# Kernel optimization log

Hardware: AMD Instinct MI355X
Metric: run time of the kernel (lower is better)

Reference implementation:

```python
import jax, jax.numpy as jnp
import numpy as np

D_MODEL = 128
NEG_INF = -1e30


def setup_inputs() -> dict:
    key = jax.random.key(0)
    k1, k2, k3, k4 = jax.random.split(key, 4)
    B, Lc, Lq, d = 32, 2048, 256, D_MODEL
    C = jax.random.normal(k1, (B, Lc, d), dtype=jnp.float32)
    Q = jax.random.normal(k2, (B, Lq, d), dtype=jnp.float32)
    # Linear(3d, 1): weight laid out for cat order (Q_, C_, C_*Q_)
    w = jax.random.normal(k3, (3 * d,), dtype=jnp.float32) / np.sqrt(3 * d)
    b = jax.random.normal(k4, (1,), dtype=jnp.float32) * 0.01
    c_mask = jnp.ones((B, Lc), dtype=jnp.int32)
    q_mask = jnp.ones((B, Lq), dtype=jnp.int32)
    return {"C": C, "Q": Q, "w": w, "b": b, "c_mask": c_mask, "q_mask": q_mask}


def reference(C, Q, w, b, c_mask, q_mask):
    d = C.shape[-1]
    # Algebraic decomposition of Linear([Q_, C_, C_*Q_]) -> scalar:
    # S[b,i,j] = Q[b,j]@w_q + C[b,i]@w_c + (C[b,i]*w_m)@Q[b,j] + bias
    w_q, w_c, w_m = w[:d], w[d:2 * d], w[2 * d:]
    S = (C @ w_c)[:, :, None] \
        + (Q @ w_q)[:, None, :] \
        + jnp.einsum('bid,bjd->bij', C * w_m, Q) \
        + b[0]                                        # (B, Lc, Lq)
    mask = (c_mask[:, :, None] * q_mask[:, None, :]).astype(S.dtype)
    S = S * mask + NEG_INF * (1.0 - mask)
    S1 = jax.nn.softmax(S, axis=1)  # softmax over context dim (as in source)
    S2 = jax.nn.softmax(S, axis=2)  # softmax over query dim
    C2Q = jnp.einsum('bij,bjd->bid', S1, Q)           # (B, Lc, d)
    # Q2C = S1 @ S2^T @ C, associated as S1 @ (S2^T @ C) to avoid (Lc,Lc)
    T = jnp.einsum('bkj,bkd->bjd', S2, C)             # (B, Lq, d)
    Q2C = jnp.einsum('bij,bjd->bid', S1, T)           # (B, Lc, d)
    out = jnp.concatenate([C, C2Q, C * C2Q, C * Q2C], axis=2)  # (B, Lc, 4d)
    # dropout omitted (deterministic reference / eval mode)
    return out
```

## Files before the change

kernel.cpp:

```cpp
#include <hip/hip_runtime.h>


#define BB   32
#define LC   2048
#define LQ   256
#define DM   128
#define NEG_INF_F (-1e30f)

using bf16x8  = __attribute__((ext_vector_type(8))) __bf16;
using f32x4   = __attribute__((ext_vector_type(4))) float;
using ushort8 = __attribute__((ext_vector_type(8))) unsigned short;

__device__ __forceinline__ unsigned short f2bf(float x) {
    unsigned int u = __float_as_uint(x);
    u += 0x7fffu + ((u >> 16) & 1u);
    return (unsigned short)(u >> 16);
}
__device__ __forceinline__ float bf2f(unsigned short h) {
    return __uint_as_float(((unsigned int)h) << 16);
}
__device__ __forceinline__ f32x4 mfma16(bf16x8 a, bf16x8 b, f32x4 c) {
    return __builtin_amdgcn_mfma_f32_16x16x32_bf16(a, b, c, 0, 0, 0);
}

__global__ __launch_bounds__(256) void k_tr(const float* __restrict__ src,
                                            unsigned short* __restrict__ dst) {
    const int b = blockIdx.z;
    const int j0 = blockIdx.x * 64;
    const int d0 = blockIdx.y * 64;
    const int tid = threadIdx.x;
    __shared__ float tile[64][65];

    const int r = tid >> 2, c0 = (tid & 3) * 16;
    const float* srow = src + (size_t)(b * LQ + j0 + r) * DM + d0 + c0;
#pragma unroll
    for (int u = 0; u < 4; ++u) {
        float4 v = ((const float4*)srow)[u];
        tile[r][c0 + u * 4 + 0] = v.x;
        tile[r][c0 + u * 4 + 1] = v.y;
        tile[r][c0 + u * 4 + 2] = v.z;
        tile[r][c0 + u * 4 + 3] = v.w;
    }
    __syncthreads();
    unsigned short o[16];
#pragma unroll
    for (int u = 0; u < 16; ++u) o[u] = f2bf(tile[c0 + u][r]);
    ushort8* dp = (ushort8*)(dst + (size_t)(b * DM + d0 + r) * LQ + j0 + c0);
    dp[0] = *(ushort8*)&o[0];
    dp[1] = *(ushort8*)&o[8];
}

__global__ __launch_bounds__(512) void k1_scores(
    const float* __restrict__ C, const float* __restrict__ Q,
    const float* __restrict__ w, const float* __restrict__ bptr,
    const int* __restrict__ c_mask, const int* __restrict__ q_mask,
    unsigned short* __restrict__ E, float* __restrict__ l1g, float* __restrict__ l2g) {
    const int b = blockIdx.y;
    const int i0 = blockIdx.x * 128;
    const int tid = threadIdx.x;
    const int lane = tid & 63, wid = tid >> 6;
    const int quad = lane >> 4, l15 = lane & 15;

    __shared__ unsigned short Alds[128][136];
    __shared__ unsigned short Qlds[256][136];
    __shared__ float wsm[384];
    __shared__ float rcs[128], rqs[256];
    __shared__ float cms[128], qms[256];
    __shared__ float l1s[256], l2s[128];
    __shared__ float b0s;

    if (tid < 384) wsm[tid] = w[tid];
    if (tid == 0) b0s = bptr[0];
    if (tid < 128) { cms[tid] = (float)c_mask[b * LC + i0 + tid]; l2s[tid] = 0.f; }
    if (tid < 256) { qms[tid] = (float)q_mask[b * LQ + tid]; l1s[tid] = 0.f; }
    __syncthreads();

    {
        const int r = tid >> 2, qq = tid & 3;
        const float* crow = C + (size_t)(b * LC + i0 + r) * DM + qq * 32;
        float prc = 0.f;
#pragma unroll
        for (int u = 0; u < 8; ++u) {
            float4 v = ((const float4*)crow)[u];
            int c0 = qq * 32 + u * 4;
            prc += v.x * wsm[128 + c0] + v.y * wsm[129 + c0] +
                   v.z * wsm[130 + c0] + v.w * wsm[131 + c0];
            Alds[r][c0 + 0] = f2bf(v.x * wsm[256 + c0]);
            Alds[r][c0 + 1] = f2bf(v.y * wsm[257 + c0]);
            Alds[r][c0 + 2] = f2bf(v.z * wsm[258 + c0]);
            Alds[r][c0 + 3] = f2bf(v.w * wsm[259 + c0]);
        }
        prc += __shfl_xor(prc, 1);
        prc += __shfl_xor(prc, 2);
        if (qq == 0) rcs[r] = prc;
    }
    {
        const int r = tid >> 1, hh = tid & 1;
        const float* qrow = Q + (size_t)(b * LQ + r) * DM + hh * 64;
        float prq = 0.f;
#pragma unroll
        for (int u = 0; u < 16; ++u) {
            float4 v = ((const float4*)qrow)[u];
            int c0 = hh * 64 + u * 4;
            prq += v.x * wsm[c0] + v.y * wsm[c0 + 1] + v.z * wsm[c0 + 2] + v.w * wsm[c0 + 3];
            Qlds[r][c0 + 0] = f2bf(v.x);
            Qlds[r][c0 + 1] = f2bf(v.y);
            Qlds[r][c0 + 2] = f2bf(v.z);
            Qlds[r][c0 + 3] = f2bf(v.w);
        }
        prq += __shfl_xor(prq, 1);
        if (hh == 0) rqs[r] = prq;
    }
    __syncthreads();

    const int m_base = (wid >> 2) * 64;
    const int n_base = (wid & 3) * 64;
    const f32x4 z4 = {0.f, 0.f, 0.f, 0.f};
    f32x4 acc[4][4];
#pragma unroll
    for (int mt = 0; mt < 4; ++mt)
#pragma unroll
        for (int nt = 0; nt < 4; ++nt) acc[mt][nt] = z4;

#pragma unroll
    for (int kc = 0; kc < 4; ++kc) {
        const int ko = kc * 32 + quad * 8;
        bf16x8 af[4], bfr[4];
#pragma unroll
        for (int mt = 0; mt < 4; ++mt)
            af[mt] = *(const bf16x8*)&Alds[m_base + mt * 16 + l15][ko];
#pragma unroll
        for (int nt = 0; nt < 4; ++nt)
            bfr[nt] = *(const bf16x8*)&Qlds[n_base + nt * 16 + l15][ko];
#pragma unroll
        for (int mt = 0; mt < 4; ++mt)
#pragma unroll
            for (int nt = 0; nt < 4; ++nt)
                acc[mt][nt] = mfma16(af[mt], bfr[nt], acc[mt][nt]);
    }

    const float b0 = b0s;
    float colsum[4] = {0.f, 0.f, 0.f, 0.f};
#pragma unroll
    for (int mt = 0; mt < 4; ++mt) {
#pragma unroll
        for (int reg = 0; reg < 4; ++reg) {
            const int m = m_base + mt * 16 + quad * 4 + reg;
            float rowsum = 0.f;
#pragma unroll
            for (int nt = 0; nt < 4; ++nt) {
                const int n = n_base + nt * 16 + l15;
                float s = acc[mt][nt][reg] + rcs[m] + rqs[n] + b0;
                const float mk = cms[m] * qms[n];
                s = s * mk + NEG_INF_F * (1.f - mk);
                const float e = __expf(s);
                E[(size_t)(b * LC + i0 + m) * LQ + n] = f2bf(e);
                rowsum += e;
                colsum[nt] += e;
            }
            rowsum += __shfl_xor(rowsum, 1);
            rowsum += __shfl_xor(rowsum, 2);
            rowsum += __shfl_xor(rowsum, 4);
            rowsum += __shfl_xor(rowsum, 8);
            if (l15 == 0) atomicAdd(&l2s[m], rowsum);
        }
    }
#pragma unroll
    for (int nt = 0; nt < 4; ++nt) {
        float v = colsum[nt];
        v += __shfl_xor(v, 16);
        v += __shfl_xor(v, 32);
        if (quad == 0) atomicAdd(&l1s[n_base + nt * 16 + l15], v);
    }
    __syncthreads();
    if (tid < 128) l2g[b * LC + i0 + tid] = l2s[tid];
    if (tid < 256) atomicAdd(&l1g[b * LQ + tid], l1s[tid]);
}

__global__ __launch_bounds__(256) void k3_T(
    const unsigned short* __restrict__ E, const float* __restrict__ C,
    const float* __restrict__ l2g, float* __restrict__ T) {
    const int split = blockIdx.x;
    const int j0 = blockIdx.y * 64;
    const int b = blockIdx.z;
    const int tid = threadIdx.x;
    const int lane = tid & 63, wid = tid >> 6;
    const int quad = lane >> 4, l15 = lane & 15;
    const int ibase = split * 1024;
    const int n_base = wid * 32;

    __shared__ unsigned short At[64][72];
    __shared__ unsigned short Bt[128][72];
    __shared__ float rl2s[1024];

    for (int u = tid; u < 1024; u += 256)
        rl2s[u] = 1.0f / l2g[b * LC + ibase + u];

    const f32x4 z4 = {0.f, 0.f, 0.f, 0.f};
    f32x4 acc[4][2];
#pragma unroll
    for (int mt = 0; mt < 4; ++mt) { acc[mt][0] = z4; acc[mt][1] = z4; }

    for (int it = 0; it < 16; ++it) {
        const int ic = ibase + it * 64;
        __syncthreads();
        {
            const int ii = tid >> 2, s = (tid & 3) * 16;
            const ushort8* ep = (const ushort8*)(E + (size_t)(b * LC + ic + ii) * LQ + j0 + s);
            ushort8 e0 = ep[0], e1 = ep[1];
#pragma unroll
            for (int u = 0; u < 8; ++u) At[s + u][ii] = e0[u];
#pragma unroll
            for (int u = 0; u < 8; ++u) At[s + 8 + u][ii] = e1[u];
        }
        {
            const int ii = tid >> 2, s = (tid & 3) * 32;
            const float rl = rl2s[it * 64 + ii];
            const float4* cp = (const float4*)(C + (size_t)(b * LC + ic + ii) * DM + s);
#pragma unroll
            for (int u = 0; u < 8; ++u) {
                float4 v = cp[u];
                const int d0 = s + u * 4;
                Bt[d0 + 0][ii] = f2bf(v.x * rl);
                Bt[d0 + 1][ii] = f2bf(v.y * rl);
                Bt[d0 + 2][ii] = f2bf(v.z * rl);
                Bt[d0 + 3][ii] = f2bf(v.w * rl);
            }
        }
        __syncthreads();
#pragma unroll
        for (int kk = 0; kk < 2; ++kk) {
            const int ko = kk * 32 + quad * 8;
            bf16x8 a[4], bb[2];
#pragma unroll
            for (int mt = 0; mt < 4; ++mt)
                a[mt] = *(const bf16x8*)&At[mt * 16 + l15][ko];
#pragma unroll
            for (int nt = 0; nt < 2; ++nt)
                bb[nt] = *(const bf16x8*)&Bt[n_base + nt * 16 + l15][ko];
#pragma unroll
            for (int mt = 0; mt < 4; ++mt)
#pragma unroll
                for (int nt = 0; nt < 2; ++nt)
                    acc[mt][nt] = mfma16(a[mt], bb[nt], acc[mt][nt]);
        }
    }
#pragma unroll
    for (int mt = 0; mt < 4; ++mt)
#pragma unroll
        for (int reg = 0; reg < 4; ++reg) {
            const int j = j0 + mt * 16 + quad * 4 + reg;
#pragma unroll
            for (int nt = 0; nt < 2; ++nt) {
                const int d = n_base + nt * 16 + l15;
                atomicAdd(&T[(size_t)(b * LQ + j) * DM + d], acc[mt][nt][reg]);
            }
        }
}

__global__ __launch_bounds__(256) void k4_out(
    const unsigned short* __restrict__ E, const float* __restrict__ C,
    const unsigned short* __restrict__ Qt, const unsigned short* __restrict__ Tt,
    const float* __restrict__ l1g, float* __restrict__ out) {
    const int b = blockIdx.y;
    const int i0 = blockIdx.x * 128;
    const int tid = threadIdx.x;
    const int lane = tid & 63, wid = tid >> 6;
    const int quad = lane >> 4, l15 = lane & 15;
    const int m_base = (wid >> 1) * 64, n_base = (wid & 1) * 64;

    __shared__ unsigned short Aq[128][72];
    __shared__ unsigned short Bq[128][72];
    __shared__ unsigned short Bt2[128][72];
    __shared__ float rl1[256];

    if (tid < 256) rl1[tid] = 1.0f / l1g[b * LQ + tid];

    const f32x4 z4 = {0.f, 0.f, 0.f, 0.f};
    f32x4 acc1[4][4], acc2[4][4];
#pragma unroll
    for (int mt = 0; mt < 4; ++mt)
#pragma unroll
        for (int nt = 0; nt < 4; ++nt) { acc1[mt][nt] = z4; acc2[mt][nt] = z4; }

#pragma unroll 1
    for (int kc = 0; kc < 4; ++kc) {
        const int jc = kc * 64;
        __syncthreads();
        {
            const int r = tid >> 1, s = (tid & 1) * 32;
            const ushort8* ep = (const ushort8*)(E + (size_t)(b * LC + i0 + r) * LQ + jc + s);
            const ushort8* qp = (const ushort8*)(Qt + (size_t)(b * DM + r) * LQ + jc + s);
            const ushort8* tp = (const ushort8*)(Tt + (size_t)(b * DM + r) * LQ + jc + s);
#pragma unroll
            for (int u = 0; u < 4; ++u) {
                ushort8 ev = ep[u];
                unsigned short av[8];
#pragma unroll
                for (int q = 0; q < 8; ++q) {
                    const int jj = s + u * 8 + q;
                    av[q] = f2bf(bf2f(ev[q]) * rl1[jc + jj]);
                }
                *(ushort8*)&Aq[r][s + u * 8] = *(ushort8*)&av[0];
                *(ushort8*)&Bq[r][s + u * 8] = qp[u];
                *(ushort8*)&Bt2[r][s + u * 8] = tp[u];
            }
        }
        __syncthreads();
#pragma unroll
        for (int kk = 0; kk < 2; ++kk) {
            const int ko = kk * 32 + quad * 8;
            bf16x8 a[4], bq[4], bt[4];
#pragma unroll
            for (int mt = 0; mt < 4; ++mt)
                a[mt] = *(const bf16x8*)&Aq[m_base + mt * 16 + l15][ko];
#pragma unroll
            for (int nt = 0; nt < 4; ++nt) {
                bq[nt] = *(const bf16x8*)&Bq[n_base + nt * 16 + l15][ko];
                bt[nt] = *(const bf16x8*)&Bt2[n_base + nt * 16 + l15][ko];
            }
#pragma unroll
            for (int mt = 0; mt < 4; ++mt)
#pragma unroll
                for (int nt = 0; nt < 4; ++nt) {
                    acc1[mt][nt] = mfma16(a[mt], bq[nt], acc1[mt][nt]);
                    acc2[mt][nt] = mfma16(a[mt], bt[nt], acc2[mt][nt]);
                }
        }
    }

#pragma unroll
    for (int mt = 0; mt < 4; ++mt)
#pragma unroll
        for (int reg = 0; reg < 4; ++reg) {
            const int i = i0 + m_base + mt * 16 + quad * 4 + reg;
            const size_t rb = (size_t)(b * LC + i) * 512;
            const float* crow = C + (size_t)(b * LC + i) * DM;
#pragma unroll
            for (int nt = 0; nt < 4; ++nt) {
                const int d = n_base + nt * 16 + l15;
                const float c = crow[d];
                const float v1 = acc1[mt][nt][reg];
                const float v2 = acc2[mt][nt][reg];
                out[rb + d] = c;
                out[rb + 128 + d] = v1;
                out[rb + 256 + d] = c * v1;
                out[rb + 384 + d] = c * v2;
            }
        }
}

extern "C" void kernel_launch(void* const* d_in, const int* in_sizes, int n_in,
                              void* d_out, int out_size, void* d_ws, size_t ws_size,
                              hipStream_t stream) {
    const float* C = (const float*)d_in[0];
    const float* Q = (const float*)d_in[1];
    const float* w = (const float*)d_in[2];
    const float* bp = (const float*)d_in[3];
    const int* cm = (const int*)d_in[4];
    const int* qm = (const int*)d_in[5];
    float* out = (float*)d_out;

    char* ws = (char*)d_ws;
    unsigned short* E  = (unsigned short*)(ws);
    float*          T  = (float*)(ws + 33554432);
    float*          l1 = (float*)(ws + 37748736);
    unsigned short* Qt = (unsigned short*)(ws + 37781504);
    unsigned short* Tt = (unsigned short*)(ws + 39878656);
    float*          l2 = (float*)(ws + 41975808);

    hipMemsetAsync(ws + 33554432, 0, 4194304 + 32768, stream);

    k_tr<<<dim3(4, 2, 32), 256, 0, stream>>>(Q, Qt);
    k1_scores<<<dim3(16, 32), 512, 0, stream>>>(C, Q, w, bp, cm, qm, E, l1, l2);
    k3_T<<<dim3(2, 4, 32), 256, 0, stream>>>(E, C, l2, T);
    k_tr<<<dim3(4, 2, 32), 256, 0, stream>>>(T, Tt);
    k4_out<<<dim3(16, 32), 256, 0, stream>>>(E, C, Qt, Tt, l1, out);
}
```

Before: 269.0 us.

## Restructure attention pipeline: pre-normalize scores, pretranspose C, drop T atomics

Scores are now stored already divided by their row sums. The column normalization moves into a pre-scaled transposed Q and into the T output, and k4 multiplies by the row sum to recover S1. Q is preprocessed once into bf16 row-major and transposed copies along with its w_q projection, and C is pretransposed to bf16. This lets the T kernel run as a plain tiled GEMM that writes the bf16 transposed result directly, replacing split-K float atomics and a separate transpose. The score and output kernels use smaller 64-row tiles to launch more blocks. In exchange it adds an extra full pass over C and two more small kernels.

```diff
diff --git a/kernel.cpp b/kernel.cpp
--- a/kernel.cpp
+++ b/kernel.cpp
@@ -1,10 +1,9 @@
 #include <hip/hip_runtime.h>
 
 
-#define BB   32
-#define LC   2048
-#define LQ   256
-#define DM   128
+#define LC 2048
+#define LQ 256
+#define DM 128
 #define NEG_INF_F (-1e30f)
 
 using bf16x8  = __attribute__((ext_vector_type(8))) __bf16;
@@ -23,98 +22,119 @@
     return __builtin_amdgcn_mfma_f32_16x16x32_bf16(a, b, c, 0, 0, 0);
 }
 
-__global__ __launch_bounds__(256) void k_tr(const float* __restrict__ src,
-                                            unsigned short* __restrict__ dst) {
-    const int b = blockIdx.z;
-    const int j0 = blockIdx.x * 64;
-    const int d0 = blockIdx.y * 64;
+__global__ __launch_bounds__(256) void k_preQ(const float* __restrict__ Q,
+        const float* __restrict__ w, unsigned short* __restrict__ Qbf,
+        unsigned short* __restrict__ Qt, float* __restrict__ rq) {
+    const int b = blockIdx.z, j0 = blockIdx.x * 64, d0 = blockIdx.y * 64;
     const int tid = threadIdx.x;
     __shared__ float tile[64][65];
-
+    __shared__ float wq[128];
+    if (tid < 128) wq[tid] = w[tid];
+    __syncthreads();
     const int r = tid >> 2, c0 = (tid & 3) * 16;
-    const float* srow = src + (size_t)(b * LQ + j0 + r) * DM + d0 + c0;
+    const float4* sp = (const float4*)(Q + (size_t)(b * LQ + j0 + r) * DM + d0 + c0);
+    float v[16];
 #pragma unroll
     for (int u = 0; u < 4; ++u) {
-        float4 v = ((const float4*)srow)[u];
-        tile[r][c0 + u * 4 + 0] = v.x;
-        tile[r][c0 + u * 4 + 1] = v.y;
-        tile[r][c0 + u * 4 + 2] = v.z;
-        tile[r][c0 + u * 4 + 3] = v.w;
-    }
+        float4 t = sp[u];
+        v[4*u] = t.x; v[4*u+1] = t.y; v[4*u+2] = t.z; v[4*u+3] = t.w;
+    }
+    unsigned short ob[16];
+    float p = 0.f;
+#pragma unroll
+    for (int u = 0; u < 16; ++u) {
+        ob[u] = f2bf(v[u]);
+        p += v[u] * wq[d0 + c0 + u];
+        tile[r][c0 + u] = v[u];
+    }
+    ushort8* qb = (ushort8*)(Qbf + (size_t)(b * LQ + j0 + r) * DM + d0 + c0);
+    qb[0] = *(ushort8*)&ob[0];
+    qb[1] = *(ushort8*)&ob[8];
+    p += __shfl_xor(p, 1);
+    p += __shfl_xor(p, 2);
+    if ((tid & 3) == 0) atomicAdd(&rq[b * LQ + j0 + r], p);
     __syncthreads();
     unsigned short o[16];
 #pragma unroll
     for (int u = 0; u < 16; ++u) o[u] = f2bf(tile[c0 + u][r]);
-    ushort8* dp = (ushort8*)(dst + (size_t)(b * DM + d0 + r) * LQ + j0 + c0);
+    ushort8* dp = (ushort8*)(Qt + (size_t)(b * DM + d0 + r) * LQ + j0 + c0);
     dp[0] = *(ushort8*)&o[0];
     dp[1] = *(ushort8*)&o[8];
 }
 
-__global__ __launch_bounds__(512) void k1_scores(
-    const float* __restrict__ C, const float* __restrict__ Q,
+__global__ __launch_bounds__(256) void k_preC(const float* __restrict__ C,
+        unsigned short* __restrict__ Ct) {
+    const int b = blockIdx.z, i0 = blockIdx.x * 64, d0 = blockIdx.y * 64;
+    const int tid = threadIdx.x;
+    __shared__ float tile[64][65];
+    const int r = tid >> 2, c0 = (tid & 3) * 16;
+    const float4* sp = (const float4*)(C + (size_t)(b * LC + i0 + r) * DM + d0 + c0);
+#pragma unroll
+    for (int u = 0; u < 4; ++u) {
+        float4 t = sp[u];
+        tile[r][c0 + 4*u] = t.x; tile[r][c0 + 4*u + 1] = t.y;
+        tile[r][c0 + 4*u + 2] = t.z; tile[r][c0 + 4*u + 3] = t.w;
+    }
+    __syncthreads();
+    unsigned short o[16];
+#pragma unroll
+    for (int u = 0; u < 16; ++u) o[u] = f2bf(tile[c0 + u][r]);
+    ushort8* dp = (ushort8*)(Ct + (size_t)(b * DM + d0 + r) * LC + i0 + c0);
+    dp[0] = *(ushort8*)&o[0];
+    dp[1] = *(ushort8*)&o[8];
+}
+
+__global__ __launch_bounds__(256) void k1_scores(
+    const float* __restrict__ C, const unsigned short* __restrict__ Qbf,
     const float* __restrict__ w, const float* __restrict__ bptr,
     const int* __restrict__ c_mask, const int* __restrict__ q_mask,
+    const float* __restrict__ rq,
     unsigned short* __restrict__ E, float* __restrict__ l1g, float* __restrict__ l2g) {
     const int b = blockIdx.y;
-    const int i0 = blockIdx.x * 128;
+    const int i0 = blockIdx.x * 64;
     const int tid = threadIdx.x;
     const int lane = tid & 63, wid = tid >> 6;
     const int quad = lane >> 4, l15 = lane & 15;
 
-    __shared__ unsigned short Alds[128][136];
-    __shared__ unsigned short Qlds[256][136];
-    __shared__ float wsm[384];
-    __shared__ float rcs[128], rqs[256];
-    __shared__ float cms[128], qms[256];
-    __shared__ float l1s[256], l2s[128];
+    __shared__ unsigned short Alds[64][136];
+    __shared__ float wsm[256];
+    __shared__ float rcs[64], rqs[256], cms[64], qms[256], l2s[64];
     __shared__ float b0s;
 
-    if (tid < 384) wsm[tid] = w[tid];
+    if (tid < 256) {
+        wsm[tid] = w[128 + tid];
+        rqs[tid] = rq[b * LQ + tid];
+        qms[tid] = (float)q_mask[b * LQ + tid];
+    }
+    if (tid < 64) {
+        cms[tid] = (float)c_mask[b * LC + i0 + tid];
+        l2s[tid] = 0.f;
+    }
     if (tid == 0) b0s = bptr[0];
-    if (tid < 128) { cms[tid] = (float)c_mask[b * LC + i0 + tid]; l2s[tid] = 0.f; }
-    if (tid < 256) { qms[tid] = (float)q_mask[b * LQ + tid]; l1s[tid] = 0.f; }
     __syncthreads();
 
     {
         const int r = tid >> 2, qq = tid & 3;
-        const float* crow = C + (size_t)(b * LC + i0 + r) * DM + qq * 32;
+        const float4* cp = (const float4*)(C + (size_t)(b * LC + i0 + r) * DM + qq * 32);
         float prc = 0.f;
 #pragma unroll
         for (int u = 0; u < 8; ++u) {
-            float4 v = ((const float4*)crow)[u];
-            int c0 = qq * 32 + u * 4;
-            prc += v.x * wsm[128 + c0] + v.y * wsm[129 + c0] +
-                   v.z * wsm[130 + c0] + v.w * wsm[131 + c0];
-            Alds[r][c0 + 0] = f2bf(v.x * wsm[256 + c0]);
-            Alds[r][c0 + 1] = f2bf(v.y * wsm[257 + c0]);
-            Alds[r][c0 + 2] = f2bf(v.z * wsm[258 + c0]);
-            Alds[r][c0 + 3] = f2bf(v.w * wsm[259 + c0]);
+            float4 v = cp[u];
+            const int c0 = qq * 32 + u * 4;
+            prc += v.x * wsm[c0] + v.y * wsm[c0 + 1] + v.z * wsm[c0 + 2] + v.w * wsm[c0 + 3];
+            Alds[r][c0 + 0] = f2bf(v.x * wsm[128 + c0]);
+            Alds[r][c0 + 1] = f2bf(v.y * wsm[129 + c0]);
+            Alds[r][c0 + 2] = f2bf(v.z * wsm[130 + c0]);
+            Alds[r][c0 + 3] = f2bf(v.w * wsm[131 + c0]);
         }
         prc += __shfl_xor(prc, 1);
         prc += __shfl_xor(prc, 2);
         if (qq == 0) rcs[r] = prc;
     }
-    {
-        const int r = tid >> 1, hh = tid & 1;
-        const float* qrow = Q + (size_t)(b * LQ + r) * DM + hh * 64;
-        float prq = 0.f;
-#pragma unroll
-        for (int u = 0; u < 16; ++u) {
-            float4 v = ((const float4*)qrow)[u];
-            int c0 = hh * 64 + u * 4;
-            prq += v.x * wsm[c0] + v.y * wsm[c0 + 1] + v.z * wsm[c0 + 2] + v.w * wsm[c0 + 3];
-            Qlds[r][c0 + 0] = f2bf(v.x);
-            Qlds[r][c0 + 1] = f2bf(v.y);
-            Qlds[r][c0 + 2] = f2bf(v.z);
-            Qlds[r][c0 + 3] = f2bf(v.w);
-        }
-        prq += __shfl_xor(prq, 1);
-        if (hh == 0) rqs[r] = prq;
-    }
-    __syncthreads();
-
-    const int m_base = (wid >> 2) * 64;
-    const int n_base = (wid & 3) * 64;
+    __syncthreads();
+
+    const int n_base = wid * 64;
+    const unsigned short* qbase = Qbf + (size_t)b * LQ * DM;
     const f32x4 z4 = {0.f, 0.f, 0.f, 0.f};
     f32x4 acc[4][4];
 #pragma unroll
@@ -128,10 +148,10 @@
         bf16x8 af[4], bfr[4];
 #pragma unroll
         for (int mt = 0; mt < 4; ++mt)
-            af[mt] = *(const bf16x8*)&Alds[m_base + mt * 16 + l15][ko];
+            af[mt] = *(const bf16x8*)&Alds[mt * 16 + l15][ko];
 #pragma unroll
         for (int nt = 0; nt < 4; ++nt)
-            bfr[nt] = *(const bf16x8*)&Qlds[n_base + nt * 16 + l15][ko];
+            bfr[nt] = *(const bf16x8*)(qbase + (size_t)(n_base + nt * 16 + l15) * DM + ko);
 #pragma unroll
         for (int mt = 0; mt < 4; ++mt)
 #pragma unroll
@@ -145,7 +165,7 @@
     for (int mt = 0; mt < 4; ++mt) {
 #pragma unroll
         for (int reg = 0; reg < 4; ++reg) {
-            const int m = m_base + mt * 16 + quad * 4 + reg;
+            const int m = mt * 16 + quad * 4 + reg;
             float rowsum = 0.f;
 #pragma unroll
             for (int nt = 0; nt < 4; ++nt) {
@@ -154,7 +174,7 @@
                 const float mk = cms[m] * qms[n];
                 s = s * mk + NEG_INF_F * (1.f - mk);
                 const float e = __expf(s);
-                E[(size_t)(b * LC + i0 + m) * LQ + n] = f2bf(e);
+                acc[mt][nt][reg] = e;
                 rowsum += e;
                 colsum[nt] += e;
             }
@@ -170,159 +190,161 @@
         float v = colsum[nt];
         v += __shfl_xor(v, 16);
         v += __shfl_xor(v, 32);
-        if (quad == 0) atomicAdd(&l1s[n_base + nt * 16 + l15], v);
-    }
-    __syncthreads();
-    if (tid < 128) l2g[b * LC + i0 + tid] = l2s[tid];
-    if (tid < 256) atomicAdd(&l1g[b * LQ + tid], l1s[tid]);
-}
-
-__global__ __launch_bounds__(256) void k3_T(
-    const unsigned short* __restrict__ E, const float* __restrict__ C,
-    const float* __restrict__ l2g, float* __restrict__ T) {
-    const int split = blockIdx.x;
-    const int j0 = blockIdx.y * 64;
-    const int b = blockIdx.z;
+        if (quad == 0) atomicAdd(&l1g[b * LQ + n_base + nt * 16 + l15], v);
+    }
+    __syncthreads();
+    if (tid < 64) l2g[b * LC + i0 + tid] = l2s[tid];
+
+#pragma unroll
+    for (int mt = 0; mt < 4; ++mt) {
+#pragma unroll
+        for (int reg = 0; reg < 4; ++reg) {
+            const int m = mt * 16 + quad * 4 + reg;
+            const float rl = 1.0f / l2s[m];
+            unsigned short* erow = E + (size_t)(b * LC + i0 + m) * LQ;
+#pragma unroll
+            for (int nt = 0; nt < 4; ++nt) {
+                const int n = n_base + nt * 16 + l15;
+                erow[n] = f2bf(acc[mt][nt][reg] * rl);
+            }
+        }
+    }
+}
+
+__global__ __launch_bounds__(256) void kS_scaleQt(
+    const unsigned short* __restrict__ Qt, const float* __restrict__ l1g,
+    unsigned short* __restrict__ Qts) {
+    const int b = blockIdx.y;
+    const int tid = threadIdx.x;
+    __shared__ float rl1s[256];
+    rl1s[tid] = 1.0f / l1g[b * LQ + tid];
+    __syncthreads();
+    const int idx = blockIdx.x * 256 + tid;
+    const int d = idx >> 5, jc = (idx & 31) * 8;
+    const ushort8 v = *(const ushort8*)(Qt + (size_t)(b * DM + d) * LQ + jc);
+    unsigned short o[8];
+#pragma unroll
+    for (int u = 0; u < 8; ++u) o[u] = f2bf(bf2f(v[u]) * rl1s[jc + u]);
+    *(ushort8*)(Qts + (size_t)(b * DM + d) * LQ + jc) = *(ushort8*)&o[0];
+}
+
+__global__ __launch_bounds__(512) void k3_Tt(
+    const unsigned short* __restrict__ E, const unsigned short* __restrict__ Ct,
+    const float* __restrict__ l1g, unsigned short* __restrict__ Tt) {
+    const int j0 = blockIdx.x * 64, d0 = blockIdx.y * 64, b = blockIdx.z;
     const int tid = threadIdx.x;
     const int lane = tid & 63, wid = tid >> 6;
     const int quad = lane >> 4, l15 = lane & 15;
-    const int ibase = split * 1024;
-    const int n_base = wid * 32;
-
-    __shared__ unsigned short At[64][72];
-    __shared__ unsigned short Bt[128][72];
-    __shared__ float rl2s[1024];
-
-    for (int u = tid; u < 1024; u += 256)
-        rl2s[u] = 1.0f / l2g[b * LC + ibase + u];
+    const int m_base = (wid >> 1) * 16, n32 = (wid & 1) * 32;
+
+    __shared__ unsigned short Ab[64][136];
+    __shared__ unsigned short Bb[64][136];
+    __shared__ float rl1s[64];
+    if (tid < 64) rl1s[tid] = 1.0f / l1g[b * LQ + j0 + tid];
 
     const f32x4 z4 = {0.f, 0.f, 0.f, 0.f};
-    f32x4 acc[4][2];
-#pragma unroll
-    for (int mt = 0; mt < 4; ++mt) { acc[mt][0] = z4; acc[mt][1] = z4; }
+    f32x4 acc[2] = {z4, z4};
 
     for (int it = 0; it < 16; ++it) {
-        const int ic = ibase + it * 64;
+        const int ic = it * 128;
         __syncthreads();
         {
-            const int ii = tid >> 2, s = (tid & 3) * 16;
-            const ushort8* ep = (const ushort8*)(E + (size_t)(b * LC + ic + ii) * LQ + j0 + s);
+            const int r = tid >> 3, q = tid & 7;
+            const ushort8* cp = (const ushort8*)(Ct + (size_t)(b * DM + d0 + r) * LC + ic + q * 16);
+            *(ushort8*)&Ab[r][q * 16] = cp[0];
+            *(ushort8*)&Ab[r][q * 16 + 8] = cp[1];
+        }
+        {
+            const int il = tid >> 2, sg = (tid & 3) * 16;
+            const ushort8* ep = (const ushort8*)(E + (size_t)(b * LC + ic + il) * LQ + j0 + sg);
             ushort8 e0 = ep[0], e1 = ep[1];
 #pragma unroll
-            for (int u = 0; u < 8; ++u) At[s + u][ii] = e0[u];
-#pragma unroll
-            for (int u = 0; u < 8; ++u) At[s + 8 + u][ii] = e1[u];
-        }
-        {
-            const int ii = tid >> 2, s = (tid & 3) * 32;
-            const float rl = rl2s[it * 64 + ii];
-            const float4* cp = (const float4*)(C + (size_t)(b * LC + ic + ii) * DM + s);
-#pragma unroll
-            for (int u = 0; u < 8; ++u) {
-                float4 v = cp[u];
-                const int d0 = s + u * 4;
-                Bt[d0 + 0][ii] = f2bf(v.x * rl);
-                Bt[d0 + 1][ii] = f2bf(v.y * rl);
-                Bt[d0 + 2][ii] = f2bf(v.z * rl);
-                Bt[d0 + 3][ii] = f2bf(v.w * rl);
-            }
+            for (int u = 0; u < 8; ++u) Bb[sg + u][il] = e0[u];
+#pragma unroll
+            for (int u = 0; u < 8; ++u) Bb[sg + 8 + u][il] = e1[u];
         }
         __syncthreads();
 #pragma unroll
-        for (int kk = 0; kk < 2; ++kk) {
+        for (int kk = 0; kk < 4; ++kk) {
             const int ko = kk * 32 + quad * 8;
-            bf16x8 a[4], bb[2];
-#pragma unroll
-            for (int mt = 0; mt < 4; ++mt)
-                a[mt] = *(const bf16x8*)&At[mt * 16 + l15][ko];
-#pragma unroll
-            for (int nt = 0; nt < 2; ++nt)
-                bb[nt] = *(const bf16x8*)&Bt[n_base + nt * 16 + l15][ko];
-#pragma unroll
-            for (int mt = 0; mt < 4; ++mt)
-#pragma unroll
-                for (int nt = 0; nt < 2; ++nt)
-                    acc[mt][nt] = mfma16(a[mt], bb[nt], acc[mt][nt]);
-        }
-    }
-#pragma unroll
-    for (int mt = 0; mt < 4; ++mt)
+            bf16x8 af = *(const bf16x8*)&Ab[m_base + l15][ko];
+            bf16x8 b0f = *(const bf16x8*)&Bb[n32 + l15][ko];
+            bf16x8 b1f = *(const bf16x8*)&Bb[n32 + 16 + l15][ko];
+            acc[0] = mfma16(af, b0f, acc[0]);
+            acc[1] = mfma16(af, b1f, acc[1]);
+        }
+    }
+#pragma unroll
+    for (int nt = 0; nt < 2; ++nt)
 #pragma unroll
         for (int reg = 0; reg < 4; ++reg) {
-            const int j = j0 + mt * 16 + quad * 4 + reg;
-#pragma unroll
-            for (int nt = 0; nt < 2; ++nt) {
-                const int d = n_base + nt * 16 + l15;
-                atomicAdd(&T[(size_t)(b * LQ + j) * DM + d], acc[mt][nt][reg]);
-            }
+            const int dd = d0 + m_base + quad * 4 + reg;
+            const int jl = n32 + nt * 16 + l15;
+            Tt[(size_t)(b * DM + dd) * LQ + j0 + jl] = f2bf(acc[nt][reg] * rl1s[jl]);
         }
 }
 
 __global__ __launch_bounds__(256) void k4_out(
     const unsigned short* __restrict__ E, const float* __restrict__ C,
-    const unsigned short* __restrict__ Qt, const unsigned short* __restrict__ Tt,
-    const float* __restrict__ l1g, float* __restrict__ out) {
+    const unsigned short* __restrict__ Qts, const unsigned short* __restrict__ Tt,
+    const float* __restrict__ l2g, float* __restrict__ out) {
     const int b = blockIdx.y;
-    const int i0 = blockIdx.x * 128;
+    const int i0 = blockIdx.x * 64;
     const int tid = threadIdx.x;
     const int lane = tid & 63, wid = tid >> 6;
     const int quad = lane >> 4, l15 = lane & 15;
-    const int m_base = (wid >> 1) * 64, n_base = (wid & 1) * 64;
-
-    __shared__ unsigned short Aq[128][72];
+    const int n_base = wid * 32;
+
+    __shared__ unsigned short Aq[64][72];
     __shared__ unsigned short Bq[128][72];
     __shared__ unsigned short Bt2[128][72];
-    __shared__ float rl1[256];
-
-    if (tid < 256) rl1[tid] = 1.0f / l1g[b * LQ + tid];
+    __shared__ float l2s[64];
+    if (tid < 64) l2s[tid] = l2g[b * LC + i0 + tid];
 
     const f32x4 z4 = {0.f, 0.f, 0.f, 0.f};
-    f32x4 acc1[4][4], acc2[4][4];
+    f32x4 acc1[4][2], acc2[4][2];
 #pragma unroll
     for (int mt = 0; mt < 4; ++mt)
 #pragma unroll
-        for (int nt = 0; nt < 4; ++nt) { acc1[mt][nt] = z4; acc2[mt][nt] = z4; }
+        for (int nt = 0; nt < 2; ++nt) { acc1[mt][nt] = z4; acc2[mt][nt] = z4; }
 
 #pragma unroll 1
     for (int kc = 0; kc < 4; ++kc) {
         const int jc = kc * 64;
         __syncthreads();
         {
-            const int r = tid >> 1, s = (tid & 1) * 32;
-            const ushort8* ep = (const ushort8*)(E + (size_t)(b * LC + i0 + r) * LQ + jc + s);
-            const ushort8* qp = (const ushort8*)(Qt + (size_t)(b * DM + r) * LQ + jc + s);
-            const ushort8* tp = (const ushort8*)(Tt + (size_t)(b * DM + r) * LQ + jc + s);
+            const int r = tid >> 2, q = tid & 3;
+            const ushort8* ep = (const ushort8*)(E + (size_t)(b * LC + i0 + r) * LQ + jc + q * 16);
+            *(ushort8*)&Aq[r][q * 16] = ep[0];
+            *(ushort8*)&Aq[r][q * 16 + 8] = ep[1];
+        }
+        {
+            const int r = tid >> 1, h = (tid & 1) * 32;
+            const ushort8* qp = (const ushort8*)(Qts + (size_t)(b * DM + r) * LQ + jc + h);
+            const ushort8* tp = (const ushort8*)(Tt + (size_t)(b * DM + r) * LQ + jc + h);
 #pragma unroll
             for (int u = 0; u < 4; ++u) {
-                ushort8 ev = ep[u];
-                unsigned short av[8];
-#pragma unroll
-                for (int q = 0; q < 8; ++q) {
-                    const int jj = s + u * 8 + q;
-                    av[q] = f2bf(bf2f(ev[q]) * rl1[jc + jj]);
-                }
-                *(ushort8*)&Aq[r][s + u * 8] = *(ushort8*)&av[0];
-                *(ushort8*)&Bq[r][s + u * 8] = qp[u];
-                *(ushort8*)&Bt2[r][s + u * 8] = tp[u];
+                *(ushort8*)&Bq[r][h + u * 8] = qp[u];
+                *(ushort8*)&Bt2[r][h + u * 8] = tp[u];
             }
         }
         __syncthreads();
 #pragma unroll
         for (int kk = 0; kk < 2; ++kk) {
             const int ko = kk * 32 + quad * 8;
-            bf16x8 a[4], bq[4], bt[4];
+            bf16x8 a[4], bq[2], bt[2];
 #pragma unroll
             for (int mt = 0; mt < 4; ++mt)
-                a[mt] = *(const bf16x8*)&Aq[m_base + mt * 16 + l15][ko];
-#pragma unroll
-            for (int nt = 0; nt < 4; ++nt) {
+                a[mt] = *(const bf16x8*)&Aq[mt * 16 + l15][ko];
+#pragma unroll
+            for (int nt = 0; nt < 2; ++nt) {
                 bq[nt] = *(const bf16x8*)&Bq[n_base + nt * 16 + l15][ko];
                 bt[nt] = *(const bf16x8*)&Bt2[n_base + nt * 16 + l15][ko];
             }
 #pragma unroll
             for (int mt = 0; mt < 4; ++mt)
 #pragma unroll
-                for (int nt = 0; nt < 4; ++nt) {
+                for (int nt = 0; nt < 2; ++nt) {
                     acc1[mt][nt] = mfma16(a[mt], bq[nt], acc1[mt][nt]);
                     acc2[mt][nt] = mfma16(a[mt], bt[nt], acc2[mt][nt]);
                 }
@@ -333,15 +355,17 @@
     for (int mt = 0; mt < 4; ++mt)
 #pragma unroll
         for (int reg = 0; reg < 4; ++reg) {
-            const int i = i0 + m_base + mt * 16 + quad * 4 + reg;
+            const int il = mt * 16 + quad * 4 + reg;
+            const int i = i0 + il;
+            const float l2v = l2s[il];
             const size_t rb = (size_t)(b * LC + i) * 512;
             const float* crow = C + (size_t)(b * LC + i) * DM;
 #pragma unroll
-            for (int nt = 0; nt < 4; ++nt) {
+            for (int nt = 0; nt < 2; ++nt) {
                 const int d = n_base + nt * 16 + l15;
                 const float c = crow[d];
-                const float v1 = acc1[mt][nt][reg];
-                const float v2 = acc2[mt][nt][reg];
+                const float v1 = acc1[mt][nt][reg] * l2v;
+                const float v2 = acc2[mt][nt][reg] * l2v;
                 out[rb + d] = c;
                 out[rb + 128 + d] = v1;
                 out[rb + 256 + d] = c * v1;
@@ -362,18 +386,22 @@
     float* out = (float*)d_out;
 
     char* ws = (char*)d_ws;
-    unsigned short* E  = (unsigned short*)(ws);
-    float*          T  = (float*)(ws + 33554432);
-    float*          l1 = (float*)(ws + 37748736);
-    unsigned short* Qt = (unsigned short*)(ws + 37781504);
-    unsigned short* Tt = (unsigned short*)(ws + 39878656);
-    float*          l2 = (float*)(ws + 41975808);
-
-    hipMemsetAsync(ws + 33554432, 0, 4194304 + 32768, stream);
-
-    k_tr<<<dim3(4, 2, 32), 256, 0, stream>>>(Q, Qt);
-    k1_scores<<<dim3(16, 32), 512, 0, stream>>>(C, Q, w, bp, cm, qm, E, l1, l2);
-    k3_T<<<dim3(2, 4, 32), 256, 0, stream>>>(E, C, l2, T);
-    k_tr<<<dim3(4, 2, 32), 256, 0, stream>>>(T, Tt);
-    k4_out<<<dim3(16, 32), 256, 0, stream>>>(E, C, Qt, Tt, l1, out);
-}
+    unsigned short* E   = (unsigned short*)(ws);
+    unsigned short* Ct  = (unsigned short*)(ws + 33554432);
+    unsigned short* Qbf = (unsigned short*)(ws + 50331648);
+    unsigned short* Qt  = (unsigned short*)(ws + 52428800);
+    unsigned short* Qts = (unsigned short*)(ws + 54525952);
+    unsigned short* Tt  = (unsigned short*)(ws + 56623104);
+    float*          l2g = (float*)(ws + 58720256);
+    float*          rq  = (float*)(ws + 58982400);
+    float*          l1  = (float*)(ws + 59015168);
+
+    hipMemsetAsync(ws + 58982400, 0, 65536, stream);
+
+    k_preQ<<<dim3(4, 2, 32), 256, 0, stream>>>(Q, w, Qbf, Qt, rq);
+    k_preC<<<dim3(32, 2, 32), 256, 0, stream>>>(C, Ct);
+    k1_scores<<<dim3(32, 32), 256, 0, stream>>>(C, Qbf, w, bp, cm, qm, rq, E, l1, l2g);
+    kS_scaleQt<<<dim3(16, 32), 256, 0, stream>>>(Qt, l1, Qts);
+    k3_Tt<<<dim3(4, 2, 32), 512, 0, stream>>>(E, Ct, l1, Tt);
+    k4_out<<<dim3(32, 32), 256, 0, stream>>>(E, C, Qts, Tt, l2g, out);
+}
```

New measurement: 257.0 us. 1.05x faster.
